# Kernel tuning notes

Hardware: AMD Instinct MI355X
Metric: run time of the kernel (lower is better)

Reference implementation:

```python
import jax, jax.numpy as jnp
import numpy as np

D_MODEL = 1024
NUM_HEADS = 16
DIM_KEY = D_MODEL // NUM_HEADS
B, S = 2, 2048


def setup_inputs() -> dict:
    key = jax.random.key(0)
    ks = jax.random.split(key, 11)
    s = 1.0 / np.sqrt(D_MODEL)
    inp = {
        "query": jax.random.normal(ks[0], (B, S, D_MODEL), jnp.float32),
        "key": jax.random.normal(ks[1], (B, S, D_MODEL), jnp.float32),
        "value": jax.random.normal(ks[2], (B, S, D_MODEL), jnp.float32),
        "W_q": jax.random.uniform(ks[3], (D_MODEL, D_MODEL), jnp.float32, -s, s),
        "b_q": jax.random.uniform(ks[4], (D_MODEL,), jnp.float32, -s, s),
        "W_k": jax.random.uniform(ks[5], (D_MODEL, D_MODEL), jnp.float32, -s, s),
        "b_k": jax.random.uniform(ks[6], (D_MODEL,), jnp.float32, -s, s),
        "W_v": jax.random.uniform(ks[7], (D_MODEL, D_MODEL), jnp.float32, -s, s),
        "b_v": jax.random.uniform(ks[8], (D_MODEL,), jnp.float32, -s, s),
        "W_o": jax.random.uniform(ks[9], (D_MODEL, D_MODEL), jnp.float32, -s, s),
        "b_o": jax.random.uniform(ks[10], (D_MODEL,), jnp.float32, -s, s),
    }
    return inp


def _split_heads(x):
    # [B, S, D] -> [B, H, S, dk]
    b, s, _ = x.shape
    return x.reshape(b, s, NUM_HEADS, DIM_KEY).transpose(0, 2, 1, 3)


def reference(query, key, value, W_q, b_q, W_k, b_k, W_v, b_v, W_o, b_o):
    # torch Linear: y = x @ W^T + b
    q = _split_heads(query @ W_q.T + b_q)   # [B,H,S,dk]
    k = _split_heads(key @ W_k.T + b_k)
    v = _split_heads(value @ W_v.T + b_v)
    scale = 1.0 / np.sqrt(DIM_KEY).astype(np.float32)
    scores = jnp.einsum("bhqd,bhkd->bhqk", q, k) * scale  # [B,H,S,S]
    probs = jax.nn.softmax(scores, axis=-1)
    attn = jnp.einsum("bhqk,bhkd->bhqd", probs, v)        # [B,H,S,dk]
    combined = attn.transpose(0, 2, 1, 3).reshape(query.shape[0], query.shape[1], D_MODEL)
    return combined @ W_o.T + b_o
```

## Files before the change

kernel.cpp:

```cpp
#include <hip/hip_runtime.h>
#include <stdint.h>


typedef float f32x4 __attribute__((ext_vector_type(4)));
typedef __bf16 bf16x8 __attribute__((ext_vector_type(8)));
typedef unsigned short u16;

__device__ __forceinline__ u16 f2bf(float x){
  unsigned u = __float_as_uint(x);
  u += 0x7fffu + ((u>>16)&1u);
  return (u16)(u>>16);
}
__device__ __forceinline__ unsigned cvt_pk_bf16(float a, float b){
  unsigned r;
  asm("v_cvt_pk_bf16_f32 %0, %1, %2" : "=v"(r) : "v"(a), "v"(b));
  return r;
}
__device__ __forceinline__ void glds16(const void* g, void* l){
  __builtin_amdgcn_global_load_lds((__attribute__((address_space(1))) void*)g,
                                   (__attribute__((address_space(3))) void*)l, 16, 0, 0);
}
#define MFMA16(a,b,c) __builtin_amdgcn_mfma_f32_16x16x32_bf16(a,b,c,0,0,0)

__global__ __launch_bounds__(256) void cvt_all(
    const float* __restrict__ q, const float* __restrict__ k, const float* __restrict__ v,
    const float* __restrict__ wq, const float* __restrict__ wk, const float* __restrict__ wv,
    const float* __restrict__ wo, u16* __restrict__ ws)
{
  size_t g = ((size_t)blockIdx.x*256 + threadIdx.x)*4;
  int seg = (int)(g >> 20);
  const float* src; size_t base;
  if      (seg <  4){ src=q;  base=(size_t)0u;       }
  else if (seg <  8){ src=k;  base=(size_t)4u<<20;   }
  else if (seg < 12){ src=v;  base=(size_t)8u<<20;   }
  else if (seg ==12){ src=wq; base=(size_t)12u<<20;  }
  else if (seg ==13){ src=wk; base=(size_t)13u<<20;  }
  else if (seg ==14){ src=wv; base=(size_t)14u<<20;  }
  else              { src=wo; base=(size_t)15u<<20;  }
  float4 val = *(const float4*)(src + (g - base));
  uint2 o; o.x = cvt_pk_bf16(val.x, val.y); o.y = cvt_pk_bf16(val.z, val.w);
  *(uint2*)(ws + g) = o;
}

template<int MODE>
__device__ __forceinline__ void gemm128_core(const u16* __restrict__ A, const u16* __restrict__ Wt,
                                             const float* __restrict__ bias, u16* __restrict__ outB,
                                             float scale)
{
  __shared__ __align__(16) u16 As[128*32];
  __shared__ __align__(16) u16 Bs[128*32];
  const int tid  = threadIdx.x;
  const int lane = tid & 63, w = tid >> 6;
  const int quad = lane >> 4, l15 = lane & 15;
  const int m0 = blockIdx.y*128, n0 = blockIdx.x*128;
  const int wm = (w>>1)*64, wn = (w&1)*64;
  const int sw = (l15>>1)&3;

  f32x4 acc[4][4];
  #pragma unroll
  for (int i=0;i<4;i++)
    #pragma unroll
    for (int j=0;j<4;j++) acc[i][j] = (f32x4){0.f,0.f,0.f,0.f};

  for (int kt = 0; kt < 1024; kt += 32){
    #pragma unroll
    for (int t=0;t<2;t++){
      int id = t*256 + tid;
      int r = id>>2;
      int gc = (id&3) ^ ((id>>3)&3);
      glds16(A  + (size_t)(m0+r)*1024 + kt + gc*8, (void*)&As[id*8]);
      glds16(Wt + (size_t)(n0+r)*1024 + kt + gc*8, (void*)&Bs[id*8]);
    }
    __syncthreads();
    bf16x8 af[4], bfv[4];
    #pragma unroll
    for (int i=0;i<4;i++) af[i]  = *(const bf16x8*)&As[(wm + i*16 + l15)*32 + (quad^sw)*8];
    #pragma unroll
    for (int j=0;j<4;j++) bfv[j] = *(const bf16x8*)&Bs[(wn + j*16 + l15)*32 + (quad^sw)*8];
    #pragma unroll
    for (int i=0;i<4;i++)
      #pragma unroll
      for (int j=0;j<4;j++)
        acc[i][j] = MFMA16(af[i], bfv[j], acc[i][j]);
    __syncthreads();
  }

  if (MODE == 2){
    #pragma unroll
    for (int i=0;i<4;i++)
      #pragma unroll
      for (int j=0;j<4;j++){
        int row = m0 + wm + i*16 + quad*4;
        int col = n0 + wn + j*16 + l15;
        float bc = bias[col];
        uint2 pk;
        pk.x = cvt_pk_bf16(acc[i][j][0]+bc, acc[i][j][1]+bc);
        pk.y = cvt_pk_bf16(acc[i][j][2]+bc, acc[i][j][3]+bc);
        int bh = ((row>>11)<<4) + (col>>6);
        size_t o = ((size_t)bh*64 + (col&63))*2048 + (row&2047);
        *(uint2*)(outB + o) = pk;
      }
  } else {
    #pragma unroll
    for (int i=0;i<4;i++)
      #pragma unroll
      for (int j=0;j<4;j++)
        #pragma unroll
        for (int r=0;r<4;r++){
          int row = m0 + wm + i*16 + quad*4 + r;
          int col = n0 + wn + j*16 + l15;
          float vv = (acc[i][j][r] + bias[col]) * scale;
          size_t o = ((size_t)((row>>11)*16 + (col>>6))*2048 + (row&2047))*64 + (col&63);
          outB[o] = f2bf(vv);
        }
  }
}

__global__ __launch_bounds__(256,3) void gemm_qkv(
  const u16* __restrict__ Xq, const u16* __restrict__ Xk, const u16* __restrict__ Xv,
  const u16* __restrict__ Wq, const u16* __restrict__ Wk, const u16* __restrict__ Wv,
  const float* __restrict__ bq, const float* __restrict__ bk, const float* __restrict__ bv,
  u16* __restrict__ Qh, u16* __restrict__ Kh, u16* __restrict__ Vt)
{
  const int z = blockIdx.z;
  if (z == 2){
    gemm128_core<2>(Xv, Wv, bv, Vt, 1.0f);
  } else if (z == 1){
    gemm128_core<0>(Xk, Wk, bk, Kh, 1.0f);
  } else {
    gemm128_core<0>(Xq, Wq, bq, Qh, 0.1803368801111243f);
  }
}

__global__ __launch_bounds__(256,2) void gemm_out(
  const u16* __restrict__ comb, const u16* __restrict__ Wo,
  const float* __restrict__ bo, float* __restrict__ out)
{
  __shared__ __align__(16) u16 As[64*32];
  __shared__ __align__(16) u16 Bs[128*32];
  const int tid  = threadIdx.x;
  const int lane = tid & 63, w = tid >> 6;
  const int quad = lane >> 4, l15 = lane & 15;
  const int m0 = blockIdx.y*64, n0 = blockIdx.x*128;
  const int sw = (l15>>1)&3;

  f32x4 acc[4][2];
  #pragma unroll
  for (int i=0;i<4;i++)
    #pragma unroll
    for (int j=0;j<2;j++) acc[i][j] = (f32x4){0.f,0.f,0.f,0.f};

  for (int kt = 0; kt < 1024; kt += 32){
    {
      int id = tid;
      int r = id>>2;
      int gc = (id&3) ^ ((id>>3)&3);
      glds16(comb + (size_t)(m0+r)*1024 + kt + gc*8, (void*)&As[id*8]);
    }
    #pragma unroll
    for (int t=0;t<2;t++){
      int id = t*256 + tid;
      int r = id>>2;
      int gc = (id&3) ^ ((id>>3)&3);
      glds16(Wo + (size_t)(n0+r)*1024 + kt + gc*8, (void*)&Bs[id*8]);
    }
    __syncthreads();
    bf16x8 af[4], bfv[2];
    #pragma unroll
    for (int i=0;i<4;i++) af[i]  = *(const bf16x8*)&As[(i*16 + l15)*32 + (quad^sw)*8];
    #pragma unroll
    for (int j=0;j<2;j++) bfv[j] = *(const bf16x8*)&Bs[(w*32 + j*16 + l15)*32 + (quad^sw)*8];
    #pragma unroll
    for (int i=0;i<4;i++)
      #pragma unroll
      for (int j=0;j<2;j++)
        acc[i][j] = MFMA16(af[i], bfv[j], acc[i][j]);
    __syncthreads();
  }

  #pragma unroll
  for (int i=0;i<4;i++)
    #pragma unroll
    for (int j=0;j<2;j++)
      #pragma unroll
      for (int r=0;r<4;r++){
        int row = m0 + i*16 + quad*4 + r;
        int col = n0 + w*32 + j*16 + l15;
        out[(size_t)row*1024 + col] = acc[i][j][r] + bo[col];
      }
}

__global__ __launch_bounds__(256,2) void attn(
  const u16* __restrict__ Q, const u16* __restrict__ K, const u16* __restrict__ Vt,
  u16* __restrict__ comb)
{
  __shared__ __align__(16) u16 K_s[128*64];
  __shared__ __align__(16) u16 V_s[64*128];
  __shared__ __align__(16) u16 P_s[128*128];
  const int tid = threadIdx.x;
  const int lane = tid&63, w = tid>>6, quad = lane>>4, l15 = lane&15;
  const int l7 = l15&7;
  const int bh = blockIdx.y, q0 = blockIdx.x*128;
  const u16* Qb = Q  + ((size_t)bh*2048 + q0)*64;
  const u16* Kb = K  + (size_t)bh*2048*64;
  const u16* Vb = Vt + (size_t)bh*64*2048;

  #pragma unroll
  for (int it=0; it<4; it++){
    int id = it*256 + tid;
    int gc = (id&7) ^ ((id>>3)&7);
    glds16(Qb + (size_t)(id>>3)*64 + gc*8, (void*)&P_s[id*8]);
  }
  __syncthreads();
  bf16x8 qa[2][2];
  #pragma unroll
  for (int c2=0; c2<2; c2++)
    #pragma unroll
    for (int ks=0; ks<2; ks++)
      qa[c2][ks] = *(const bf16x8*)&P_s[(w*32 + c2*16 + l15)*64 + ((ks*4+quad)^l7)*8];
  __syncthreads();

  const __bf16 one1 = (__bf16)1.0f;
  const bf16x8 ones = (bf16x8){one1,one1,one1,one1,one1,one1,one1,one1};

  f32x4 O[2][4];
  #pragma unroll
  for (int rt=0; rt<2; rt++)
    #pragma unroll
    for (int dt=0; dt<4; dt++) O[rt][dt] = (f32x4){0.f,0.f,0.f,0.f};
  f32x4 lacc[2] = {(f32x4){0.f,0.f,0.f,0.f}, (f32x4){0.f,0.f,0.f,0.f}};

  for (int t=0; t<16; t++){
    const int kv0 = t*128;
    #pragma unroll
    for (int it=0; it<4; it++){
      int id = it*256 + tid;
      int gck = (id&7)  ^ ((id>>3)&7);
      int gcv = (id&15) ^ ((id>>4)&15);
      glds16(Kb + (size_t)(kv0 + (id>>3))*64 + gck*8, (void*)&K_s[id*8]);
      glds16(Vb + (size_t)(id>>4)*2048 + kv0 + gcv*8, (void*)&V_s[id*8]);
    }
    __syncthreads();

    #pragma unroll
    for (int r8=0; r8<8; r8++){
      bf16x8 ka0 = *(const bf16x8*)&K_s[(r8*16 + l15)*64 + ((0+quad)^l7)*8];
      bf16x8 ka1 = *(const bf16x8*)&K_s[(r8*16 + l15)*64 + ((4+quad)^l7)*8];
      #pragma unroll
      for (int c2=0; c2<2; c2++){
        f32x4 s = (f32x4){0.f,0.f,0.f,0.f};
        s = MFMA16(ka0, qa[c2][0], s);
        s = MFMA16(ka1, qa[c2][1], s);
        int qq   = w*32 + c2*16 + l15;
        int chnk = (r8*2 + (quad>>1)) ^ l15;
        int off  = qq*128 + chnk*8 + (quad&1)*4;
        uint2 pw;
        pw.x = cvt_pk_bf16(__builtin_amdgcn_exp2f(s[0]), __builtin_amdgcn_exp2f(s[1]));
        pw.y = cvt_pk_bf16(__builtin_amdgcn_exp2f(s[2]), __builtin_amdgcn_exp2f(s[3]));
        *(uint2*)&P_s[off] = pw;
      }
    }

    bf16x8 pa[2][4];
    #pragma unroll
    for (int rt=0; rt<2; rt++)
      #pragma unroll
      for (int kk=0; kk<4; kk++){
        int qq   = w*32 + rt*16 + l15;
        int chnk = (kk*4 + quad) ^ l15;
        pa[rt][kk] = *(const bf16x8*)&P_s[qq*128 + chnk*8];
      }
    #pragma unroll
    for (int kk=0; kk<4; kk++){
      lacc[0] = MFMA16(pa[0][kk], ones, lacc[0]);
      lacc[1] = MFMA16(pa[1][kk], ones, lacc[1]);
    }
    #pragma unroll
    for (int dt=0; dt<4; dt++)
      #pragma unroll
      for (int kk=0; kk<4; kk++){
        bf16x8 vb = *(const bf16x8*)&V_s[(dt*16 + l15)*128 + (((kk*4+quad)^l15))*8];
        O[0][dt] = MFMA16(pa[0][kk], vb, O[0][dt]);
        O[1][dt] = MFMA16(pa[1][kk], vb, O[1][dt]);
      }
    __syncthreads();
  }

  const int b = bh>>4, h = bh&15;
  #pragma unroll
  for (int rt=0; rt<2; rt++)
    #pragma unroll
    for (int i=0;i<4;i++){
      float inv = 1.0f/lacc[rt][i];
      int qrow  = q0 + w*32 + rt*16 + quad*4 + i;
      #pragma unroll
      for (int dt=0; dt<4; dt++){
        size_t o = ((size_t)b*2048 + qrow)*1024 + (size_t)h*64 + dt*16 + l15;
        comb[o] = f2bf(O[rt][dt][i] * inv);
      }
    }
}

extern "C" void kernel_launch(void* const* d_in, const int* in_sizes, int n_in,
                              void* d_out, int out_size, void* d_ws, size_t ws_size,
                              hipStream_t stream)
{
  const float* q  = (const float*)d_in[0];
  const float* k  = (const float*)d_in[1];
  const float* v  = (const float*)d_in[2];
  const float* Wq = (const float*)d_in[3];
  const float* bq = (const float*)d_in[4];
  const float* Wk = (const float*)d_in[5];
  const float* bk = (const float*)d_in[6];
  const float* Wv = (const float*)d_in[7];
  const float* bv = (const float*)d_in[8];
  const float* Wo = (const float*)d_in[9];
  const float* bo = (const float*)d_in[10];
  float* out = (float*)d_out;

  u16* ws  = (u16*)d_ws;
  u16* Xq  = ws;
  u16* Xk  = ws + ((size_t)4u<<20);
  u16* Xv  = ws + ((size_t)8u<<20);
  u16* Wqb = ws + ((size_t)12u<<20);
  u16* Wkb = ws + ((size_t)13u<<20);
  u16* Wvb = ws + ((size_t)14u<<20);
  u16* Wob = ws + ((size_t)15u<<20);
  u16* Qh  = ws + ((size_t)16u<<20);
  u16* Kh  = ws + ((size_t)20u<<20);
  u16* Vt  = ws + ((size_t)24u<<20);
  u16* comb = Xq;

  cvt_all<<<16384, 256, 0, stream>>>(q, k, v, Wq, Wk, Wv, Wo, ws);
  gemm_qkv<<<dim3(8,32,3), 256, 0, stream>>>(Xq, Xk, Xv, Wqb, Wkb, Wvb, bq, bk, bv, Qh, Kh, Vt);
  attn<<<dim3(16,32), 256, 0, stream>>>(Qh, Kh, Vt, comb);
  gemm_out<<<dim3(8,64), 256, 0, stream>>>(comb, Wob, bo, out);
}
```

Before: 223.0 us.

## Split attention KV tile across wave pairs with 64-row query blocks

Attention blocks now cover 64 query rows instead of 128, which doubles the grid. The four waves are split into two query halves times two KV halves, and the partial O and row-sum accumulators are reduced through shared memory at the end. P_s shrinks so occupancy can rise to three blocks per CU. The cost is that K/V tiles are loaded twice as often per query row, plus an extra reduction step.

```diff
diff --git a/kernel.cpp b/kernel.cpp
--- a/kernel.cpp
+++ b/kernel.cpp
@@ -190,23 +190,25 @@
       }
 }
 
-__global__ __launch_bounds__(256,2) void attn(
+__global__ __launch_bounds__(256,3) void attn(
   const u16* __restrict__ Q, const u16* __restrict__ K, const u16* __restrict__ Vt,
   u16* __restrict__ comb)
 {
   __shared__ __align__(16) u16 K_s[128*64];
   __shared__ __align__(16) u16 V_s[64*128];
-  __shared__ __align__(16) u16 P_s[128*128];
+  __shared__ __align__(16) u16 P_s[64*128];
   const int tid = threadIdx.x;
   const int lane = tid&63, w = tid>>6, quad = lane>>4, l15 = lane&15;
   const int l7 = l15&7;
-  const int bh = blockIdx.y, q0 = blockIdx.x*128;
+  const int wq = w&1;
+  const int wk = w>>1;
+  const int bh = blockIdx.y, q0 = blockIdx.x*64;
   const u16* Qb = Q  + ((size_t)bh*2048 + q0)*64;
   const u16* Kb = K  + (size_t)bh*2048*64;
   const u16* Vb = Vt + (size_t)bh*64*2048;
 
   #pragma unroll
-  for (int it=0; it<4; it++){
+  for (int it=0; it<2; it++){
     int id = it*256 + tid;
     int gc = (id&7) ^ ((id>>3)&7);
     glds16(Qb + (size_t)(id>>3)*64 + gc*8, (void*)&P_s[id*8]);
@@ -217,7 +219,7 @@
   for (int c2=0; c2<2; c2++)
     #pragma unroll
     for (int ks=0; ks<2; ks++)
-      qa[c2][ks] = *(const bf16x8*)&P_s[(w*32 + c2*16 + l15)*64 + ((ks*4+quad)^l7)*8];
+      qa[c2][ks] = *(const bf16x8*)&P_s[(wq*32 + c2*16 + l15)*64 + ((ks*4+quad)^l7)*8];
   __syncthreads();
 
   const __bf16 one1 = (__bf16)1.0f;
@@ -243,16 +245,17 @@
     __syncthreads();
 
     #pragma unroll
-    for (int r8=0; r8<8; r8++){
-      bf16x8 ka0 = *(const bf16x8*)&K_s[(r8*16 + l15)*64 + ((0+quad)^l7)*8];
-      bf16x8 ka1 = *(const bf16x8*)&K_s[(r8*16 + l15)*64 + ((4+quad)^l7)*8];
+    for (int r8=0; r8<4; r8++){
+      int krow = wk*64 + r8*16 + l15;
+      bf16x8 ka0 = *(const bf16x8*)&K_s[krow*64 + ((0+quad)^l7)*8];
+      bf16x8 ka1 = *(const bf16x8*)&K_s[krow*64 + ((4+quad)^l7)*8];
       #pragma unroll
       for (int c2=0; c2<2; c2++){
         f32x4 s = (f32x4){0.f,0.f,0.f,0.f};
         s = MFMA16(ka0, qa[c2][0], s);
         s = MFMA16(ka1, qa[c2][1], s);
-        int qq   = w*32 + c2*16 + l15;
-        int chnk = (r8*2 + (quad>>1)) ^ l15;
+        int qq   = wq*32 + c2*16 + l15;
+        int chnk = (wk*8 + r8*2 + (quad>>1)) ^ l15;
         int off  = qq*128 + chnk*8 + (quad&1)*4;
         uint2 pw;
         pw.x = cvt_pk_bf16(__builtin_amdgcn_exp2f(s[0]), __builtin_amdgcn_exp2f(s[1]));
@@ -261,44 +264,71 @@
       }
     }
 
-    bf16x8 pa[2][4];
+    bf16x8 pa[2][2];
     #pragma unroll
     for (int rt=0; rt<2; rt++)
       #pragma unroll
-      for (int kk=0; kk<4; kk++){
-        int qq   = w*32 + rt*16 + l15;
-        int chnk = (kk*4 + quad) ^ l15;
+      for (int kk=0; kk<2; kk++){
+        int qq   = wq*32 + rt*16 + l15;
+        int chnk = (wk*8 + kk*4 + quad) ^ l15;
         pa[rt][kk] = *(const bf16x8*)&P_s[qq*128 + chnk*8];
       }
     #pragma unroll
-    for (int kk=0; kk<4; kk++){
+    for (int kk=0; kk<2; kk++){
       lacc[0] = MFMA16(pa[0][kk], ones, lacc[0]);
       lacc[1] = MFMA16(pa[1][kk], ones, lacc[1]);
     }
     #pragma unroll
     for (int dt=0; dt<4; dt++)
       #pragma unroll
-      for (int kk=0; kk<4; kk++){
-        bf16x8 vb = *(const bf16x8*)&V_s[(dt*16 + l15)*128 + (((kk*4+quad)^l15))*8];
+      for (int kk=0; kk<2; kk++){
+        bf16x8 vb = *(const bf16x8*)&V_s[(dt*16 + l15)*128 + ((wk*8 + kk*4 + quad)^l15)*8];
         O[0][dt] = MFMA16(pa[0][kk], vb, O[0][dt]);
         O[1][dt] = MFMA16(pa[1][kk], vb, O[1][dt]);
       }
     __syncthreads();
   }
 
-  const int b = bh>>4, h = bh&15;
-  #pragma unroll
-  for (int rt=0; rt<2; rt++)
-    #pragma unroll
-    for (int i=0;i<4;i++){
-      float inv = 1.0f/lacc[rt][i];
-      int qrow  = q0 + w*32 + rt*16 + quad*4 + i;
+  float* Pf = (float*)P_s;
+  float* Kf = (float*)K_s;
+  if (w >= 2){
+    int slot = (w-2)*64 + lane;
+    #pragma unroll
+    for (int rt=0; rt<2; rt++){
       #pragma unroll
       for (int dt=0; dt<4; dt++){
-        size_t o = ((size_t)b*2048 + qrow)*1024 + (size_t)h*64 + dt*16 + l15;
-        comb[o] = f2bf(O[rt][dt][i] * inv);
-      }
-    }
+        int rc = (rt*4+dt) ^ (slot&7);
+        *(f32x4*)&Pf[slot*32 + rc*4] = O[rt][dt];
+      }
+      *(f32x4*)&Kf[slot*12 + rt*4] = lacc[rt];
+    }
+  }
+  __syncthreads();
+  if (w < 2){
+    int slot = w*64 + lane;
+    #pragma unroll
+    for (int rt=0; rt<2; rt++){
+      #pragma unroll
+      for (int dt=0; dt<4; dt++){
+        int rc = (rt*4+dt) ^ (slot&7);
+        O[rt][dt] += *(const f32x4*)&Pf[slot*32 + rc*4];
+      }
+      lacc[rt] += *(const f32x4*)&Kf[slot*12 + rt*4];
+    }
+    const int b = bh>>4, h = bh&15;
+    #pragma unroll
+    for (int rt=0; rt<2; rt++)
+      #pragma unroll
+      for (int i=0;i<4;i++){
+        float inv = 1.0f/lacc[rt][i];
+        int qrow  = q0 + w*32 + rt*16 + quad*4 + i;
+        #pragma unroll
+        for (int dt=0; dt<4; dt++){
+          size_t o = ((size_t)b*2048 + qrow)*1024 + (size_t)h*64 + dt*16 + l15;
+          comb[o] = f2bf(O[rt][dt][i] * inv);
+        }
+      }
+  }
 }
 
 extern "C" void kernel_launch(void* const* d_in, const int* in_sizes, int n_in,
@@ -333,6 +363,6 @@
 
   cvt_all<<<16384, 256, 0, stream>>>(q, k, v, Wq, Wk, Wv, Wo, ws);
   gemm_qkv<<<dim3(8,32,3), 256, 0, stream>>>(Xq, Xk, Xv, Wqb, Wkb, Wvb, bq, bk, bv, Qh, Kh, Vt);
-  attn<<<dim3(16,32), 256, 0, stream>>>(Qh, Kh, Vt, comb);
+  attn<<<dim3(32,32), 256, 0, stream>>>(Qh, Kh, Vt, comb);
   gemm_out<<<dim3(8,64), 256, 0, stream>>>(comb, Wob, bo, out);
 }
```

After: 230.9 us. 1.04x slower.
